# Optimization experiments

Hardware: AMD Instinct MI355X
Metric: run time of the kernel (lower is better)

Reference implementation:

```python
import jax, jax.numpy as jnp
import numpy as np

A, B, D, H, O = 64, 4096, 50, 192, 3

def _xavier(key, shape, gain=0.5):
    fan_in, fan_out = shape[-1], shape[-2]
    limit = gain * np.sqrt(6.0 / (fan_in + fan_out))
    return jax.random.uniform(key, shape, jnp.float32, -limit, limit)

def setup_inputs() -> dict:
    key = jax.random.key(0)
    ks = jax.random.split(key, 12)
    return {
        "x": jax.random.normal(ks[0], (B, D), jnp.float32),
        "input_norm_weight": _xavier(ks[1], (A, D)),
        "input_norm_bias": jnp.zeros((A, D), jnp.float32),
        "layer1_weight": _xavier(ks[2], (A, H, D)),
        "layer1_bias": jnp.zeros((A, H), jnp.float32),
        "layer2_weight": _xavier(ks[3], (A, H, H)),
        "layer2_bias": jnp.zeros((A, H), jnp.float32),
        "layer3_weight": _xavier(ks[4], (A, H, H)),
        "layer3_bias": jnp.zeros((A, H), jnp.float32),
        "output_weight": _xavier(ks[5], (A, O, H)),
        "output_bias": jnp.zeros((A, O), jnp.float32),
        "skip1_weight": _xavier(ks[6], (A, H, D)),
        "skip1_bias": jnp.zeros((A, H), jnp.float32),
        "skip2_weight": _xavier(ks[7], (A, H, H)),
        "skip2_bias": jnp.zeros((A, H), jnp.float32),
        "hidden_norm_weight": _xavier(ks[8], (A, H)),
        "hidden_norm_bias": jnp.zeros((A, H), jnp.float32),
    }

def reference(x, input_norm_weight, input_norm_bias,
              layer1_weight, layer1_bias, layer2_weight, layer2_bias,
              layer3_weight, layer3_bias, output_weight, output_bias,
              skip1_weight, skip1_bias, skip2_weight, skip2_bias,
              hidden_norm_weight, hidden_norm_bias):
    # NOTE: the vectorized ensemble's "norms" are affine-only (no mean/var), per source.
    # x: [B, D] -> broadcast over agents: [A, B, D]
    x_norm = x[None, :, :] * input_norm_weight[:, None, :] + input_norm_bias[:, None, :]
    gelu = lambda t: jax.nn.gelu(t, approximate=False)  # torch F.gelu exact
    # per-agent GEMMs: [A,B,in] x [A,out,in] -> [A,B,out]
    h1 = gelu(jnp.einsum('abi,ahi->abh', x_norm, layer1_weight) + layer1_bias[:, None, :]) \
         + jnp.einsum('abi,ahi->abh', x_norm, skip1_weight) + skip1_bias[:, None, :]
    h2 = gelu(jnp.einsum('abi,ahi->abh', h1, layer2_weight) + layer2_bias[:, None, :]) \
         + jnp.einsum('abi,ahi->abh', h1, skip2_weight) + skip2_bias[:, None, :]
    h3 = jnp.einsum('abi,ahi->abh', h2, layer3_weight) + layer3_bias[:, None, :] + h2
    h3 = h3 * hidden_norm_weight[:, None, :] + hidden_norm_bias[:, None, :]
    logits = jnp.einsum('abh,aoh->abo', h3, output_weight) + output_bias[:, None, :]
    return logits  # [A, B, O]
```

## Files before the change

### kernel.cpp

```cpp
#include <hip/hip_runtime.h>
#include <math.h>

#define A_N 64
#define B_N 4096
#define D_N 50
#define H_N 192
#define O_N 3

typedef __attribute__((ext_vector_type(8))) __bf16 bf16x8;
typedef __attribute__((ext_vector_type(4))) __bf16 bf16x4;
typedef __attribute__((ext_vector_type(4))) float f32x4;

#define W1_OFF   0
#define S1_OFF   786432
#define W2_OFF   1572864
#define S2_OFF   3932160
#define W3_OFF   6291456
#define OW_OFF   8650752
#define WS_ELEMS 8847360

#if __has_builtin(__builtin_amdgcn_rcpf)
#define FRCP(x) __builtin_amdgcn_rcpf(x)
#else
#define FRCP(x) (1.0f / (x))
#endif
#if __has_builtin(__builtin_amdgcn_exp2f)
#define FEXP2(x) __builtin_amdgcn_exp2f(x)
#else
#define FEXP2(x) exp2f(x)
#endif

__device__ __forceinline__ float gelu_f(float xx) {
    float t  = 0.70710678118654752440f * xx;
    float at = fabsf(t);
    float k  = FRCP(fmaf(0.3275911f, at, 1.0f));
    float p  = fmaf(k, 1.061405429f, -1.453152027f);
    p = fmaf(k, p, 1.421413741f);
    p = fmaf(k, p, -0.284496736f);
    p = fmaf(k, p, 0.254829592f);
    p = p * k;
    float e  = FEXP2(t * t * -1.44269504088896340736f);
    float er = fmaf(-p, e, 1.0f);
    er = (t < 0.f) ? -er : er;
    return 0.5f * xx * (1.0f + er);
}

__global__ __launch_bounds__(256)
void prep_kernel(const float* __restrict__ w1, const float* __restrict__ s1,
                 const float* __restrict__ w2, const float* __restrict__ s2,
                 const float* __restrict__ w3, const float* __restrict__ ow,
                 __bf16* __restrict__ ws) {
    __shared__ __bf16 T[192 * 72];
    const int b   = blockIdx.x;
    const int tid = threadIdx.x;

    if (b < 384) {
        int m = b / 128;
        int r = b % 128; int a = r >> 1; int half = r & 1;
        const float* src = ((m == 0) ? w2 : (m == 1) ? s2 : w3) + (size_t)a * 36864;
        __bf16* dst = ws + ((m == 0) ? W2_OFF : (m == 1) ? S2_OFF : W3_OFF) + (size_t)a * 36864;
        for (int rc = half * 3; rc < half * 3 + 3; ++rc) {
            #pragma unroll
            for (int i = 0; i < 6; ++i) {
                int f4 = i * 256 + tid;
                int row = f4 / 48, kc = (f4 % 48) * 4;
                f32x4 v = *(const f32x4*)(src + (size_t)(rc * 32 + row) * 192 + kc);
                bf16x4 o;
                #pragma unroll
                for (int j = 0; j < 4; ++j) o[j] = (__bf16)v[j];
                *(bf16x4*)(T + row * 200 + kc) = o;
            }
            __syncthreads();
            #pragma unroll
            for (int i = 0; i < 3; ++i) {
                int fr = i * 256 + tid;
                int f = fr >> 6, lane = fr & 63;
                int ntl = f / 6, ks = f % 6;
                int n = ntl * 16 + (lane & 15), k = ks * 32 + (lane >> 4) * 8;
                bf16x8 v = *(const bf16x8*)(T + n * 200 + k);
                *(bf16x8*)(dst + ((size_t)(rc * 2 + ntl) * 6 + ks) * 512 + lane * 8) = v;
            }
            __syncthreads();
        }
    } else if (b < 512) {
        int r = b - 384; int m = r >> 6; int a = r & 63;
        const float* src = (m ? s1 : w1) + (size_t)a * 9600;
        __bf16* dst = ws + (m ? S1_OFF : W1_OFF) + (size_t)a * 12288;
        for (int e = tid; e < 192 * 72; e += 256) T[e] = (__bf16)0.f;
        __syncthreads();
        for (int e = tid; e < 9600; e += 256) {
            int row = e / 50, k = e - row * 50;
            T[row * 72 + k] = (__bf16)src[e];
        }
        __syncthreads();
        #pragma unroll
        for (int i = 0; i < 6; ++i) {
            int fr = i * 256 + tid;
            int f = fr >> 6, lane = fr & 63;
            int nt = f >> 1, ks = f & 1;
            int n = nt * 16 + (lane & 15), k = ks * 32 + (lane >> 4) * 8;
            bf16x8 v = *(const bf16x8*)(T + n * 72 + k);
            *(bf16x8*)(dst + (size_t)(nt * 2 + ks) * 512 + lane * 8) = v;
        }
    } else {
        int r = b - 512;
        #pragma unroll
        for (int i = 0; i < 8; ++i) {
            int fr = (r * 8 + i) * 256 + tid;
            int a = fr / 384, rem = fr - a * 384;
            int ks = rem >> 6, lane = rem & 63;
            int n = lane & 15, k = ks * 32 + (lane >> 4) * 8;
            bf16x8 v;
            if (n < O_N) {
                const float* p = ow + ((size_t)a * O_N + n) * H_N + k;
                f32x4 f0 = *(const f32x4*)p, f1 = *(const f32x4*)(p + 4);
                #pragma unroll
                for (int j = 0; j < 4; ++j) { v[j] = (__bf16)f0[j]; v[4 + j] = (__bf16)f1[j]; }
            } else {
                #pragma unroll
                for (int j = 0; j < 8; ++j) v[j] = (__bf16)0.f;
            }
            *(bf16x8*)(ws + OW_OFF + (size_t)a * 3072 + ks * 512 + lane * 8) = v;
        }
    }
}

#define MFMA(a, b, c) __builtin_amdgcn_mfma_f32_16x16x32_bf16((a), (b), (c), 0, 0, 0)

__global__ __launch_bounds__(256, 3)
void srek_mfma(const float* __restrict__ x,
               const float* __restrict__ inw, const float* __restrict__ inb,
               const float* __restrict__ b1,  const float* __restrict__ b2,
               const float* __restrict__ b3,  const float* __restrict__ s1b,
               const float* __restrict__ s2b, const float* __restrict__ hnw,
               const float* __restrict__ hnb, const float* __restrict__ ob,
               const __bf16* __restrict__ ws, float* __restrict__ out) {
    __shared__ __bf16 Xs[64 * 72];
    __shared__ __bf16 Hs[64 * 200];

    const int bid  = blockIdx.x;
    const int slot = bid >> 3;
    const int tile = slot & 63;
    const int a    = ((bid & 7) << 3) | (slot >> 6);
    const int row0 = tile * 64;

    const int tid  = threadIdx.x;
    const int lane = tid & 63;
    const int wv   = tid >> 6;
    const int ln   = lane & 15;
    const int quad = lane >> 4;
    const int aH   = a * H_N;
    const int c0   = wv * 48;
    const int l8   = lane * 8;
    const int f3   = wv * 3;

    const __bf16* W1 = ws + W1_OFF + (size_t)a * 12288;
    const __bf16* S1 = ws + S1_OFF + (size_t)a * 12288;
    const __bf16* W2 = ws + W2_OFF + (size_t)a * 36864;
    const __bf16* S2 = ws + S2_OFF + (size_t)a * 36864;
    const __bf16* W3 = ws + W3_OFF + (size_t)a * 36864;
    const __bf16* OWp= ws + OW_OFF + (size_t)a * 3072;

    bf16x8 nxt[6];
    f32x4 accT[12], accS[12], h2f[12];
    const f32x4 zero = {0.f, 0.f, 0.f, 0.f};

    #pragma unroll
    for (int t = 0; t < 3; ++t) {
        nxt[t]     = *(const bf16x8*)(W1 + ((f3 + t) * 2 + 0) * 512 + l8);
        nxt[3 + t] = *(const bf16x8*)(S1 + ((f3 + t) * 2 + 0) * 512 + l8);
    }

    for (int e = tid; e < 64 * 64; e += 256) {
        int r = e >> 6, k = e & 63;
        float v = 0.f;
        if (k < D_N) v = x[(size_t)(row0 + r) * D_N + k] * inw[a * D_N + k] + inb[a * D_N + k];
        Xs[r * 72 + k] = (__bf16)v;
    }

    auto compute_dual = [&](const __bf16* As, int pitch, int ks,
                            const bf16x8* cw, const bf16x8* cs) {
        #pragma unroll
        for (int mt = 0; mt < 4; ++mt) {
            bf16x8 av = *(const bf16x8*)(As + (mt * 16 + ln) * pitch + ks * 32 + quad * 8);
            #pragma unroll
            for (int t = 0; t < 3; ++t) {
                accT[mt * 3 + t] = MFMA(cw[t], av, accT[mt * 3 + t]);
                accS[mt * 3 + t] = MFMA(cs[t], av, accS[mt * 3 + t]);
            }
        }
    };
    auto compute_single = [&](int ks, const bf16x8* cw) {
        #pragma unroll
        for (int mt = 0; mt < 4; ++mt) {
            bf16x8 av = *(const bf16x8*)(Hs + (mt * 16 + ln) * 200 + ks * 32 + quad * 8);
            #pragma unroll
            for (int t = 0; t < 3; ++t)
                accT[mt * 3 + t] = MFMA(cw[t], av, accT[mt * 3 + t]);
        }
    };

    #pragma unroll
    for (int i = 0; i < 12; ++i) { accT[i] = zero; accS[i] = zero; }
    __syncthreads();

    {
        bf16x8 cw[3], cs[3];
        #pragma unroll
        for (int t = 0; t < 3; ++t) { cw[t] = nxt[t]; cs[t] = nxt[3 + t]; }
        #pragma unroll
        for (int t = 0; t < 3; ++t) {
            nxt[t]     = *(const bf16x8*)(W1 + ((f3 + t) * 2 + 1) * 512 + l8);
            nxt[3 + t] = *(const bf16x8*)(S1 + ((f3 + t) * 2 + 1) * 512 + l8);
        }
        compute_dual(Xs, 72, 0, cw, cs);
        #pragma unroll
        for (int t = 0; t < 3; ++t) { cw[t] = nxt[t]; cs[t] = nxt[3 + t]; }
        #pragma unroll
        for (int t = 0; t < 3; ++t) {
            nxt[t]     = *(const bf16x8*)(W2 + ((f3 + t) * 6 + 0) * 512 + l8);
            nxt[3 + t] = *(const bf16x8*)(S2 + ((f3 + t) * 6 + 0) * 512 + l8);
        }
        compute_dual(Xs, 72, 1, cw, cs);
    }
    #pragma unroll
    for (int t = 0; t < 3; ++t) {
        int colb = c0 + t * 16 + quad * 4;
        f32x4 bb = *(const f32x4*)(b1 + aH + colb);
        f32x4 sb = *(const f32x4*)(s1b + aH + colb);
        #pragma unroll
        for (int mt = 0; mt < 4; ++mt) {
            bf16x4 o;
            #pragma unroll
            for (int rg = 0; rg < 4; ++rg)
                o[rg] = (__bf16)(gelu_f(accT[mt * 3 + t][rg] + bb[rg]) + accS[mt * 3 + t][rg] + sb[rg]);
            *(bf16x4*)(Hs + (mt * 16 + ln) * 200 + colb) = o;
        }
    }
    #pragma unroll
    for (int i = 0; i < 12; ++i) { accT[i] = zero; accS[i] = zero; }
    __syncthreads();

    #pragma unroll
    for (int ks = 0; ks < 6; ++ks) {
        bf16x8 cw[3], cs[3];
        #pragma unroll
        for (int t = 0; t < 3; ++t) { cw[t] = nxt[t]; cs[t] = nxt[3 + t]; }
        if (ks < 5) {
            #pragma unroll
            for (int t = 0; t < 3; ++t) {
                nxt[t]     = *(const bf16x8*)(W2 + ((f3 + t) * 6 + ks + 1) * 512 + l8);
                nxt[3 + t] = *(const bf16x8*)(S2 + ((f3 + t) * 6 + ks + 1) * 512 + l8);
            }
        } else {
            #pragma unroll
            for (int t = 0; t < 3; ++t)
                nxt[t] = *(const bf16x8*)(W3 + ((f3 + t) * 6 + 0) * 512 + l8);
        }
        compute_dual(Hs, 200, ks, cw, cs);
    }
    #pragma unroll
    for (int t = 0; t < 3; ++t) {
        int colb = c0 + t * 16 + quad * 4;
        f32x4 bb = *(const f32x4*)(b2 + aH + colb);
        f32x4 sb = *(const f32x4*)(s2b + aH + colb);
        #pragma unroll
        for (int mt = 0; mt < 4; ++mt)
            #pragma unroll
            for (int rg = 0; rg < 4; ++rg)
                h2f[mt * 3 + t][rg] = gelu_f(accT[mt * 3 + t][rg] + bb[rg]) + accS[mt * 3 + t][rg] + sb[rg];
    }
    #pragma unroll
    for (int i = 0; i < 12; ++i) accT[i] = zero;
    __syncthreads();
    #pragma unroll
    for (int t = 0; t < 3; ++t) {
        int colb = c0 + t * 16 + quad * 4;
        #pragma unroll
        for (int mt = 0; mt < 4; ++mt) {
            bf16x4 o;
            #pragma unroll
            for (int rg = 0; rg < 4; ++rg) o[rg] = (__bf16)h2f[mt * 3 + t][rg];
            *(bf16x4*)(Hs + (mt * 16 + ln) * 200 + colb) = o;
        }
    }
    __syncthreads();

    bf16x8 ow6[6];
    #pragma unroll
    for (int ks = 0; ks < 6; ++ks) {
        bf16x8 cw[3];
        #pragma unroll
        for (int t = 0; t < 3; ++t) cw[t] = nxt[t];
        if (ks < 5) {
            #pragma unroll
            for (int t = 0; t < 3; ++t)
                nxt[t] = *(const bf16x8*)(W3 + ((f3 + t) * 6 + ks + 1) * 512 + l8);
        } else {
            #pragma unroll
            for (int kk = 0; kk < 6; ++kk)
                ow6[kk] = *(const bf16x8*)(OWp + kk * 512 + l8);
        }
        compute_single(ks, cw);
    }
    #pragma unroll
    for (int t = 0; t < 3; ++t) {
        int colb = c0 + t * 16 + quad * 4;
        f32x4 b3v = *(const f32x4*)(b3  + aH + colb);
        f32x4 nwv = *(const f32x4*)(hnw + aH + colb);
        f32x4 nbv = *(const f32x4*)(hnb + aH + colb);
        #pragma unroll
        for (int mt = 0; mt < 4; ++mt)
            #pragma unroll
            for (int rg = 0; rg < 4; ++rg)
                h2f[mt * 3 + t][rg] = fmaf(accT[mt * 3 + t][rg] + b3v[rg] + h2f[mt * 3 + t][rg],
                                           nwv[rg], nbv[rg]);
    }
    __syncthreads();
    #pragma unroll
    for (int t = 0; t < 3; ++t) {
        int colb = c0 + t * 16 + quad * 4;
        #pragma unroll
        for (int mt = 0; mt < 4; ++mt) {
            bf16x4 o;
            #pragma unroll
            for (int rg = 0; rg < 4; ++rg) o[rg] = (__bf16)h2f[mt * 3 + t][rg];
            *(bf16x4*)(Hs + (mt * 16 + ln) * 200 + colb) = o;
        }
    }
    __syncthreads();

    {
        f32x4 acco = zero;
        #pragma unroll
        for (int ks = 0; ks < 6; ++ks) {
            bf16x8 av = *(const bf16x8*)(Hs + (wv * 16 + ln) * 200 + ks * 32 + quad * 8);
            acco = MFMA(ow6[ks], av, acco);
        }
        if (quad == 0) {
            float* po = out + ((size_t)a * B_N + row0 + wv * 16 + ln) * O_N;
            po[0] = acco[0] + ob[a * O_N + 0];
            po[1] = acco[1] + ob[a * O_N + 1];
            po[2] = acco[2] + ob[a * O_N + 2];
        }
    }
}

extern "C" void kernel_launch(void* const* d_in, const int* in_sizes, int n_in,
                              void* d_out, int out_size, void* d_ws, size_t ws_size,
                              hipStream_t stream) {
    const float* x   = (const float*)d_in[0];
    const float* inw = (const float*)d_in[1];
    const float* inb = (const float*)d_in[2];
    const float* w1  = (const float*)d_in[3];
    const float* b1  = (const float*)d_in[4];
    const float* w2  = (const float*)d_in[5];
    const float* b2  = (const float*)d_in[6];
    const float* w3  = (const float*)d_in[7];
    const float* b3  = (const float*)d_in[8];
    const float* ow  = (const float*)d_in[9];
    const float* ob  = (const float*)d_in[10];
    const float* s1w = (const float*)d_in[11];
    const float* s1b = (const float*)d_in[12];
    const float* s2w = (const float*)d_in[13];
    const float* s2b = (const float*)d_in[14];
    const float* hnw = (const float*)d_in[15];
    const float* hnb = (const float*)d_in[16];

    __bf16* ws = (__bf16*)d_ws;

    prep_kernel<<<dim3(524), dim3(256), 0, stream>>>(w1, s1w, w2, s2w, w3, ow, ws);

    srek_mfma<<<dim3(A_N * (B_N / 64)), dim3(256), 0, stream>>>(
        x, inw, inb, b1, b2, b3, s1b, s2b, hnw, hnb, ob, ws, (float*)d_out);
}
```

Measured before the change: 246.5 us.

## Fold skip GEMMs into one accumulator set and raise occupancy to four blocks

The main kernel drops the separate accT, accS and h2f accumulator arrays and keeps a single set of 12 accumulators. It runs the main-weight pass, applies bias and GELU in place, then accumulates the skip-weight pass and the residual on top. This cuts register pressure so launch bounds can rise from 3 to 4 blocks per CU, at the cost of reading the activation fragments from LDS twice per layer. The prep kernel is also split into one block per 32-row chunk, giving more parallel blocks and dropping the inner loop and the extra barriers.

```diff
diff --git a/kernel.cpp b/kernel.cpp
--- a/kernel.cpp
+++ b/kernel.cpp
@@ -54,36 +54,35 @@
     const int b   = blockIdx.x;
     const int tid = threadIdx.x;
 
-    if (b < 384) {
-        int m = b / 128;
-        int r = b % 128; int a = r >> 1; int half = r & 1;
+    if (b < 1152) {
+        int m  = b / 384;
+        int r  = b % 384;
+        int a  = r / 6;
+        int rc = r % 6;
         const float* src = ((m == 0) ? w2 : (m == 1) ? s2 : w3) + (size_t)a * 36864;
         __bf16* dst = ws + ((m == 0) ? W2_OFF : (m == 1) ? S2_OFF : W3_OFF) + (size_t)a * 36864;
-        for (int rc = half * 3; rc < half * 3 + 3; ++rc) {
-            #pragma unroll
-            for (int i = 0; i < 6; ++i) {
-                int f4 = i * 256 + tid;
-                int row = f4 / 48, kc = (f4 % 48) * 4;
-                f32x4 v = *(const f32x4*)(src + (size_t)(rc * 32 + row) * 192 + kc);
-                bf16x4 o;
-                #pragma unroll
-                for (int j = 0; j < 4; ++j) o[j] = (__bf16)v[j];
-                *(bf16x4*)(T + row * 200 + kc) = o;
-            }
-            __syncthreads();
-            #pragma unroll
-            for (int i = 0; i < 3; ++i) {
-                int fr = i * 256 + tid;
-                int f = fr >> 6, lane = fr & 63;
-                int ntl = f / 6, ks = f % 6;
-                int n = ntl * 16 + (lane & 15), k = ks * 32 + (lane >> 4) * 8;
-                bf16x8 v = *(const bf16x8*)(T + n * 200 + k);
-                *(bf16x8*)(dst + ((size_t)(rc * 2 + ntl) * 6 + ks) * 512 + lane * 8) = v;
-            }
-            __syncthreads();
-        }
-    } else if (b < 512) {
-        int r = b - 384; int m = r >> 6; int a = r & 63;
+        #pragma unroll
+        for (int i = 0; i < 6; ++i) {
+            int f4 = i * 256 + tid;
+            int row = f4 / 48, kc = (f4 % 48) * 4;
+            f32x4 v = *(const f32x4*)(src + (size_t)(rc * 32 + row) * 192 + kc);
+            bf16x4 o;
+            #pragma unroll
+            for (int j = 0; j < 4; ++j) o[j] = (__bf16)v[j];
+            *(bf16x4*)(T + row * 200 + kc) = o;
+        }
+        __syncthreads();
+        #pragma unroll
+        for (int i = 0; i < 3; ++i) {
+            int fr = i * 256 + tid;
+            int f = fr >> 6, lane = fr & 63;
+            int ntl = f / 6, ks = f % 6;
+            int n = ntl * 16 + (lane & 15), k = ks * 32 + (lane >> 4) * 8;
+            bf16x8 v = *(const bf16x8*)(T + n * 200 + k);
+            *(bf16x8*)(dst + ((size_t)(rc * 2 + ntl) * 6 + ks) * 512 + lane * 8) = v;
+        }
+    } else if (b < 1280) {
+        int r = b - 1152; int m = r >> 6; int a = r & 63;
         const float* src = (m ? s1 : w1) + (size_t)a * 9600;
         __bf16* dst = ws + (m ? S1_OFF : W1_OFF) + (size_t)a * 12288;
         for (int e = tid; e < 192 * 72; e += 256) T[e] = (__bf16)0.f;
@@ -103,7 +102,7 @@
             *(bf16x8*)(dst + (size_t)(nt * 2 + ks) * 512 + lane * 8) = v;
         }
     } else {
-        int r = b - 512;
+        int r = b - 1280;
         #pragma unroll
         for (int i = 0; i < 8; ++i) {
             int fr = (r * 8 + i) * 256 + tid;
@@ -127,7 +126,7 @@
 
 #define MFMA(a, b, c) __builtin_amdgcn_mfma_f32_16x16x32_bf16((a), (b), (c), 0, 0, 0)
 
-__global__ __launch_bounds__(256, 3)
+__global__ __launch_bounds__(256, 4)
 void srek_mfma(const float* __restrict__ x,
                const float* __restrict__ inw, const float* __restrict__ inb,
                const float* __restrict__ b1,  const float* __restrict__ b2,
@@ -161,15 +160,56 @@
     const __bf16* W3 = ws + W3_OFF + (size_t)a * 36864;
     const __bf16* OWp= ws + OW_OFF + (size_t)a * 3072;
 
-    bf16x8 nxt[6];
-    f32x4 accT[12], accS[12], h2f[12];
+    bf16x8 nxt[3], cw[3], ow6[6];
+    f32x4 acc[12];
     const f32x4 zero = {0.f, 0.f, 0.f, 0.f};
 
-    #pragma unroll
-    for (int t = 0; t < 3; ++t) {
-        nxt[t]     = *(const bf16x8*)(W1 + ((f3 + t) * 2 + 0) * 512 + l8);
-        nxt[3 + t] = *(const bf16x8*)(S1 + ((f3 + t) * 2 + 0) * 512 + l8);
-    }
+    auto ldw3 = [&](const __bf16* base, int KS, int ks) {
+        #pragma unroll
+        for (int t = 0; t < 3; ++t)
+            nxt[t] = *(const bf16x8*)(base + ((f3 + t) * KS + ks) * 512 + l8);
+    };
+    auto take = [&]() {
+        #pragma unroll
+        for (int t = 0; t < 3; ++t) cw[t] = nxt[t];
+    };
+    auto pass = [&](const __bf16* As, int pitch, int ks) {
+        #pragma unroll
+        for (int mt = 0; mt < 4; ++mt) {
+            bf16x8 av = *(const bf16x8*)(As + (mt * 16 + ln) * pitch + ks * 32 + quad * 8);
+            #pragma unroll
+            for (int t = 0; t < 3; ++t)
+                acc[mt * 3 + t] = MFMA(cw[t], av, acc[mt * 3 + t]);
+        }
+    };
+    auto gelu_xform = [&](const float* bp, const float* sp) {
+        #pragma unroll
+        for (int t = 0; t < 3; ++t) {
+            int colb = c0 + t * 16 + quad * 4;
+            f32x4 bb = *(const f32x4*)(bp + aH + colb);
+            f32x4 sb = *(const f32x4*)(sp + aH + colb);
+            #pragma unroll
+            for (int mt = 0; mt < 4; ++mt)
+                #pragma unroll
+                for (int rg = 0; rg < 4; ++rg)
+                    acc[mt * 3 + t][rg] = gelu_f(acc[mt * 3 + t][rg] + bb[rg]) + sb[rg];
+        }
+    };
+    auto store_acc_bf16 = [&]() {
+        #pragma unroll
+        for (int t = 0; t < 3; ++t) {
+            int colb = c0 + t * 16 + quad * 4;
+            #pragma unroll
+            for (int mt = 0; mt < 4; ++mt) {
+                bf16x4 o;
+                #pragma unroll
+                for (int rg = 0; rg < 4; ++rg) o[rg] = (__bf16)acc[mt * 3 + t][rg];
+                *(bf16x4*)(Hs + (mt * 16 + ln) * 200 + colb) = o;
+            }
+        }
+    };
+
+    ldw3(W1, 2, 0);
 
     for (int e = tid; e < 64 * 64; e += 256) {
         int r = e >> 6, k = e & 63;
@@ -177,157 +217,71 @@
         if (k < D_N) v = x[(size_t)(row0 + r) * D_N + k] * inw[a * D_N + k] + inb[a * D_N + k];
         Xs[r * 72 + k] = (__bf16)v;
     }
-
-    auto compute_dual = [&](const __bf16* As, int pitch, int ks,
-                            const bf16x8* cw, const bf16x8* cs) {
-        #pragma unroll
-        for (int mt = 0; mt < 4; ++mt) {
-            bf16x8 av = *(const bf16x8*)(As + (mt * 16 + ln) * pitch + ks * 32 + quad * 8);
-            #pragma unroll
-            for (int t = 0; t < 3; ++t) {
-                accT[mt * 3 + t] = MFMA(cw[t], av, accT[mt * 3 + t]);
-                accS[mt * 3 + t] = MFMA(cs[t], av, accS[mt * 3 + t]);
-            }
-        }
-    };
-    auto compute_single = [&](int ks, const bf16x8* cw) {
-        #pragma unroll
-        for (int mt = 0; mt < 4; ++mt) {
-            bf16x8 av = *(const bf16x8*)(Hs + (mt * 16 + ln) * 200 + ks * 32 + quad * 8);
-            #pragma unroll
-            for (int t = 0; t < 3; ++t)
-                accT[mt * 3 + t] = MFMA(cw[t], av, accT[mt * 3 + t]);
-        }
-    };
-
-    #pragma unroll
-    for (int i = 0; i < 12; ++i) { accT[i] = zero; accS[i] = zero; }
-    __syncthreads();
-
-    {
-        bf16x8 cw[3], cs[3];
-        #pragma unroll
-        for (int t = 0; t < 3; ++t) { cw[t] = nxt[t]; cs[t] = nxt[3 + t]; }
-        #pragma unroll
-        for (int t = 0; t < 3; ++t) {
-            nxt[t]     = *(const bf16x8*)(W1 + ((f3 + t) * 2 + 1) * 512 + l8);
-            nxt[3 + t] = *(const bf16x8*)(S1 + ((f3 + t) * 2 + 1) * 512 + l8);
-        }
-        compute_dual(Xs, 72, 0, cw, cs);
-        #pragma unroll
-        for (int t = 0; t < 3; ++t) { cw[t] = nxt[t]; cs[t] = nxt[3 + t]; }
-        #pragma unroll
-        for (int t = 0; t < 3; ++t) {
-            nxt[t]     = *(const bf16x8*)(W2 + ((f3 + t) * 6 + 0) * 512 + l8);
-            nxt[3 + t] = *(const bf16x8*)(S2 + ((f3 + t) * 6 + 0) * 512 + l8);
-        }
-        compute_dual(Xs, 72, 1, cw, cs);
-    }
+    #pragma unroll
+    for (int i = 0; i < 12; ++i) acc[i] = zero;
+    __syncthreads();
+
+    take(); ldw3(W1, 2, 1); pass(Xs, 72, 0);
+    take(); ldw3(S1, 2, 0); pass(Xs, 72, 1);
+    gelu_xform(b1, s1b);
+    take(); ldw3(S1, 2, 1); pass(Xs, 72, 0);
+    take(); ldw3(W2, 6, 0); pass(Xs, 72, 1);
+    store_acc_bf16();
+    #pragma unroll
+    for (int i = 0; i < 12; ++i) acc[i] = zero;
+    __syncthreads();
+
+    #pragma unroll
+    for (int ks = 0; ks < 6; ++ks) {
+        take();
+        if (ks < 5) ldw3(W2, 6, ks + 1); else ldw3(S2, 6, 0);
+        pass(Hs, 200, ks);
+    }
+    gelu_xform(b2, s2b);
+    #pragma unroll
+    for (int ks = 0; ks < 6; ++ks) {
+        take();
+        if (ks < 5) ldw3(S2, 6, ks + 1); else ldw3(W3, 6, 0);
+        pass(Hs, 200, ks);
+    }
+    __syncthreads();
+    store_acc_bf16();
     #pragma unroll
     for (int t = 0; t < 3; ++t) {
         int colb = c0 + t * 16 + quad * 4;
-        f32x4 bb = *(const f32x4*)(b1 + aH + colb);
-        f32x4 sb = *(const f32x4*)(s1b + aH + colb);
-        #pragma unroll
-        for (int mt = 0; mt < 4; ++mt) {
-            bf16x4 o;
+        f32x4 b3v = *(const f32x4*)(b3 + aH + colb);
+        #pragma unroll
+        for (int mt = 0; mt < 4; ++mt)
             #pragma unroll
             for (int rg = 0; rg < 4; ++rg)
-                o[rg] = (__bf16)(gelu_f(accT[mt * 3 + t][rg] + bb[rg]) + accS[mt * 3 + t][rg] + sb[rg]);
-            *(bf16x4*)(Hs + (mt * 16 + ln) * 200 + colb) = o;
-        }
-    }
-    #pragma unroll
-    for (int i = 0; i < 12; ++i) { accT[i] = zero; accS[i] = zero; }
+                acc[mt * 3 + t][rg] += b3v[rg];
+    }
     __syncthreads();
 
     #pragma unroll
     for (int ks = 0; ks < 6; ++ks) {
-        bf16x8 cw[3], cs[3];
-        #pragma unroll
-        for (int t = 0; t < 3; ++t) { cw[t] = nxt[t]; cs[t] = nxt[3 + t]; }
-        if (ks < 5) {
-            #pragma unroll
-            for (int t = 0; t < 3; ++t) {
-                nxt[t]     = *(const bf16x8*)(W2 + ((f3 + t) * 6 + ks + 1) * 512 + l8);
-                nxt[3 + t] = *(const bf16x8*)(S2 + ((f3 + t) * 6 + ks + 1) * 512 + l8);
-            }
-        } else {
-            #pragma unroll
-            for (int t = 0; t < 3; ++t)
-                nxt[t] = *(const bf16x8*)(W3 + ((f3 + t) * 6 + 0) * 512 + l8);
-        }
-        compute_dual(Hs, 200, ks, cw, cs);
+        take();
+        if (ks < 5) ldw3(W3, 6, ks + 1);
+        else {
+            #pragma unroll
+            for (int kk = 0; kk < 6; ++kk)
+                ow6[kk] = *(const bf16x8*)(OWp + kk * 512 + l8);
+        }
+        pass(Hs, 200, ks);
     }
     #pragma unroll
     for (int t = 0; t < 3; ++t) {
         int colb = c0 + t * 16 + quad * 4;
-        f32x4 bb = *(const f32x4*)(b2 + aH + colb);
-        f32x4 sb = *(const f32x4*)(s2b + aH + colb);
-        #pragma unroll
-        for (int mt = 0; mt < 4; ++mt)
-            #pragma unroll
-            for (int rg = 0; rg < 4; ++rg)
-                h2f[mt * 3 + t][rg] = gelu_f(accT[mt * 3 + t][rg] + bb[rg]) + accS[mt * 3 + t][rg] + sb[rg];
-    }
-    #pragma unroll
-    for (int i = 0; i < 12; ++i) accT[i] = zero;
-    __syncthreads();
-    #pragma unroll
-    for (int t = 0; t < 3; ++t) {
-        int colb = c0 + t * 16 + quad * 4;
-        #pragma unroll
-        for (int mt = 0; mt < 4; ++mt) {
-            bf16x4 o;
-            #pragma unroll
-            for (int rg = 0; rg < 4; ++rg) o[rg] = (__bf16)h2f[mt * 3 + t][rg];
-            *(bf16x4*)(Hs + (mt * 16 + ln) * 200 + colb) = o;
-        }
-    }
-    __syncthreads();
-
-    bf16x8 ow6[6];
-    #pragma unroll
-    for (int ks = 0; ks < 6; ++ks) {
-        bf16x8 cw[3];
-        #pragma unroll
-        for (int t = 0; t < 3; ++t) cw[t] = nxt[t];
-        if (ks < 5) {
-            #pragma unroll
-            for (int t = 0; t < 3; ++t)
-                nxt[t] = *(const bf16x8*)(W3 + ((f3 + t) * 6 + ks + 1) * 512 + l8);
-        } else {
-            #pragma unroll
-            for (int kk = 0; kk < 6; ++kk)
-                ow6[kk] = *(const bf16x8*)(OWp + kk * 512 + l8);
-        }
-        compute_single(ks, cw);
-    }
-    #pragma unroll
-    for (int t = 0; t < 3; ++t) {
-        int colb = c0 + t * 16 + quad * 4;
-        f32x4 b3v = *(const f32x4*)(b3  + aH + colb);
         f32x4 nwv = *(const f32x4*)(hnw + aH + colb);
         f32x4 nbv = *(const f32x4*)(hnb + aH + colb);
         #pragma unroll
         for (int mt = 0; mt < 4; ++mt)
             #pragma unroll
             for (int rg = 0; rg < 4; ++rg)
-                h2f[mt * 3 + t][rg] = fmaf(accT[mt * 3 + t][rg] + b3v[rg] + h2f[mt * 3 + t][rg],
-                                           nwv[rg], nbv[rg]);
-    }
-    __syncthreads();
-    #pragma unroll
-    for (int t = 0; t < 3; ++t) {
-        int colb = c0 + t * 16 + quad * 4;
-        #pragma unroll
-        for (int mt = 0; mt < 4; ++mt) {
-            bf16x4 o;
-            #pragma unroll
-            for (int rg = 0; rg < 4; ++rg) o[rg] = (__bf16)h2f[mt * 3 + t][rg];
-            *(bf16x4*)(Hs + (mt * 16 + ln) * 200 + colb) = o;
-        }
-    }
+                acc[mt * 3 + t][rg] = fmaf(acc[mt * 3 + t][rg], nwv[rg], nbv[rg]);
+    }
+    __syncthreads();
+    store_acc_bf16();
     __syncthreads();
 
     {
@@ -369,7 +323,7 @@
 
     __bf16* ws = (__bf16*)d_ws;
 
-    prep_kernel<<<dim3(524), dim3(256), 0, stream>>>(w1, s1w, w2, s2w, w3, ow, ws);
+    prep_kernel<<<dim3(1292), dim3(256), 0, stream>>>(w1, s1w, w2, s2w, w3, ow, ws);
 
     srek_mfma<<<dim3(A_N * (B_N / 64)), dim3(256), 0, stream>>>(
         x, inw, inb, b1, b2, b3, s1b, s2b, hnw, hnb, ob, ws, (float*)d_out);
```

After: 306.5 us. +24.3%, slower.

## Store activations in MFMA fragment-major LDS layout and split prep blocks

Applied to the files above, without the earlier changes.

Xs and Hs switch from padded row-major LDS tiles to an MFMA fragment-major layout. Each lane's A-operand read becomes one contiguous 16-byte load at lane*8, which is meant to remove bank conflicts and index arithmetic in the inner MFMA loops. The epilogue writes now scatter into that fragment layout through a shared helper. Separately, the weight-prep kernel gives each 32-row chunk its own block (1292 blocks instead of 524), adding parallelism and dropping a loop and one barrier per chunk.

```diff
diff --git a/kernel.cpp b/kernel.cpp
--- a/kernel.cpp
+++ b/kernel.cpp
@@ -54,36 +54,35 @@
     const int b   = blockIdx.x;
     const int tid = threadIdx.x;
 
-    if (b < 384) {
-        int m = b / 128;
-        int r = b % 128; int a = r >> 1; int half = r & 1;
+    if (b < 1152) {
+        int m  = b / 384;
+        int r  = b % 384;
+        int a  = r / 6;
+        int rc = r % 6;
         const float* src = ((m == 0) ? w2 : (m == 1) ? s2 : w3) + (size_t)a * 36864;
         __bf16* dst = ws + ((m == 0) ? W2_OFF : (m == 1) ? S2_OFF : W3_OFF) + (size_t)a * 36864;
-        for (int rc = half * 3; rc < half * 3 + 3; ++rc) {
-            #pragma unroll
-            for (int i = 0; i < 6; ++i) {
-                int f4 = i * 256 + tid;
-                int row = f4 / 48, kc = (f4 % 48) * 4;
-                f32x4 v = *(const f32x4*)(src + (size_t)(rc * 32 + row) * 192 + kc);
-                bf16x4 o;
-                #pragma unroll
-                for (int j = 0; j < 4; ++j) o[j] = (__bf16)v[j];
-                *(bf16x4*)(T + row * 200 + kc) = o;
-            }
-            __syncthreads();
-            #pragma unroll
-            for (int i = 0; i < 3; ++i) {
-                int fr = i * 256 + tid;
-                int f = fr >> 6, lane = fr & 63;
-                int ntl = f / 6, ks = f % 6;
-                int n = ntl * 16 + (lane & 15), k = ks * 32 + (lane >> 4) * 8;
-                bf16x8 v = *(const bf16x8*)(T + n * 200 + k);
-                *(bf16x8*)(dst + ((size_t)(rc * 2 + ntl) * 6 + ks) * 512 + lane * 8) = v;
-            }
-            __syncthreads();
-        }
-    } else if (b < 512) {
-        int r = b - 384; int m = r >> 6; int a = r & 63;
+        #pragma unroll
+        for (int i = 0; i < 6; ++i) {
+            int f4 = i * 256 + tid;
+            int row = f4 / 48, kc = (f4 % 48) * 4;
+            f32x4 v = *(const f32x4*)(src + (size_t)(rc * 32 + row) * 192 + kc);
+            bf16x4 o;
+            #pragma unroll
+            for (int j = 0; j < 4; ++j) o[j] = (__bf16)v[j];
+            *(bf16x4*)(T + row * 200 + kc) = o;
+        }
+        __syncthreads();
+        #pragma unroll
+        for (int i = 0; i < 3; ++i) {
+            int fr = i * 256 + tid;
+            int f = fr >> 6, lane = fr & 63;
+            int ntl = f / 6, ks = f % 6;
+            int n = ntl * 16 + (lane & 15), k = ks * 32 + (lane >> 4) * 8;
+            bf16x8 v = *(const bf16x8*)(T + n * 200 + k);
+            *(bf16x8*)(dst + ((size_t)(rc * 2 + ntl) * 6 + ks) * 512 + lane * 8) = v;
+        }
+    } else if (b < 1280) {
+        int r = b - 1152; int m = r >> 6; int a = r & 63;
         const float* src = (m ? s1 : w1) + (size_t)a * 9600;
         __bf16* dst = ws + (m ? S1_OFF : W1_OFF) + (size_t)a * 12288;
         for (int e = tid; e < 192 * 72; e += 256) T[e] = (__bf16)0.f;
@@ -103,7 +102,7 @@
             *(bf16x8*)(dst + (size_t)(nt * 2 + ks) * 512 + lane * 8) = v;
         }
     } else {
-        int r = b - 512;
+        int r = b - 1280;
         #pragma unroll
         for (int i = 0; i < 8; ++i) {
             int fr = (r * 8 + i) * 256 + tid;
@@ -135,8 +134,8 @@
                const float* __restrict__ s2b, const float* __restrict__ hnw,
                const float* __restrict__ hnb, const float* __restrict__ ob,
                const __bf16* __restrict__ ws, float* __restrict__ out) {
-    __shared__ __bf16 Xs[64 * 72];
-    __shared__ __bf16 Hs[64 * 200];
+    __shared__ __bf16 Xs[8 * 512];
+    __shared__ __bf16 Hs[24 * 512];
 
     const int bid  = blockIdx.x;
     const int slot = bid >> 3;
@@ -171,18 +170,24 @@
         nxt[3 + t] = *(const bf16x8*)(S1 + ((f3 + t) * 2 + 0) * 512 + l8);
     }
 
-    for (int e = tid; e < 64 * 64; e += 256) {
-        int r = e >> 6, k = e & 63;
+    for (int e = tid; e < 8 * 512; e += 256) {
+        int j   = e & 7;
+        int lnn = (e >> 3) & 15;
+        int qd  = (e >> 7) & 3;
+        int kss = (e >> 9) & 1;
+        int mtt = (e >> 10) & 3;
+        int r = mtt * 16 + lnn;
+        int k = kss * 32 + qd * 8 + j;
         float v = 0.f;
         if (k < D_N) v = x[(size_t)(row0 + r) * D_N + k] * inw[a * D_N + k] + inb[a * D_N + k];
-        Xs[r * 72 + k] = (__bf16)v;
-    }
-
-    auto compute_dual = [&](const __bf16* As, int pitch, int ks,
+        Xs[e] = (__bf16)v;
+    }
+
+    auto compute_dual = [&](const __bf16* As, int KS, int ks,
                             const bf16x8* cw, const bf16x8* cs) {
         #pragma unroll
         for (int mt = 0; mt < 4; ++mt) {
-            bf16x8 av = *(const bf16x8*)(As + (mt * 16 + ln) * pitch + ks * 32 + quad * 8);
+            bf16x8 av = *(const bf16x8*)(As + (mt * KS + ks) * 512 + l8);
             #pragma unroll
             for (int t = 0; t < 3; ++t) {
                 accT[mt * 3 + t] = MFMA(cw[t], av, accT[mt * 3 + t]);
@@ -193,10 +198,25 @@
     auto compute_single = [&](int ks, const bf16x8* cw) {
         #pragma unroll
         for (int mt = 0; mt < 4; ++mt) {
-            bf16x8 av = *(const bf16x8*)(Hs + (mt * 16 + ln) * 200 + ks * 32 + quad * 8);
+            bf16x8 av = *(const bf16x8*)(Hs + (mt * 6 + ks) * 512 + l8);
             #pragma unroll
             for (int t = 0; t < 3; ++t)
                 accT[mt * 3 + t] = MFMA(cw[t], av, accT[mt * 3 + t]);
+        }
+    };
+    auto store_fragmajor = [&](const f32x4* src) {
+        #pragma unroll
+        for (int t = 0; t < 3; ++t) {
+            int ks2 = (3 * wv + t) >> 1;
+            int qp  = (6 * wv + 2 * t + (quad >> 1)) & 3;
+            int off = (qp * 16 + ln) * 8 + (quad & 1) * 4;
+            #pragma unroll
+            for (int mt = 0; mt < 4; ++mt) {
+                bf16x4 o;
+                #pragma unroll
+                for (int rg = 0; rg < 4; ++rg) o[rg] = (__bf16)src[mt * 3 + t][rg];
+                *(bf16x4*)(Hs + (mt * 6 + ks2) * 512 + off) = o;
+            }
         }
     };
 
@@ -213,7 +233,7 @@
             nxt[t]     = *(const bf16x8*)(W1 + ((f3 + t) * 2 + 1) * 512 + l8);
             nxt[3 + t] = *(const bf16x8*)(S1 + ((f3 + t) * 2 + 1) * 512 + l8);
         }
-        compute_dual(Xs, 72, 0, cw, cs);
+        compute_dual(Xs, 2, 0, cw, cs);
         #pragma unroll
         for (int t = 0; t < 3; ++t) { cw[t] = nxt[t]; cs[t] = nxt[3 + t]; }
         #pragma unroll
@@ -221,7 +241,7 @@
             nxt[t]     = *(const bf16x8*)(W2 + ((f3 + t) * 6 + 0) * 512 + l8);
             nxt[3 + t] = *(const bf16x8*)(S2 + ((f3 + t) * 6 + 0) * 512 + l8);
         }
-        compute_dual(Xs, 72, 1, cw, cs);
+        compute_dual(Xs, 2, 1, cw, cs);
     }
     #pragma unroll
     for (int t = 0; t < 3; ++t) {
@@ -229,14 +249,12 @@
         f32x4 bb = *(const f32x4*)(b1 + aH + colb);
         f32x4 sb = *(const f32x4*)(s1b + aH + colb);
         #pragma unroll
-        for (int mt = 0; mt < 4; ++mt) {
-            bf16x4 o;
+        for (int mt = 0; mt < 4; ++mt)
             #pragma unroll
             for (int rg = 0; rg < 4; ++rg)
-                o[rg] = (__bf16)(gelu_f(accT[mt * 3 + t][rg] + bb[rg]) + accS[mt * 3 + t][rg] + sb[rg]);
-            *(bf16x4*)(Hs + (mt * 16 + ln) * 200 + colb) = o;
-        }
-    }
+                h2f[mt * 3 + t][rg] = gelu_f(accT[mt * 3 + t][rg] + bb[rg]) + accS[mt * 3 + t][rg] + sb[rg];
+    }
+    store_fragmajor(h2f);
     #pragma unroll
     for (int i = 0; i < 12; ++i) { accT[i] = zero; accS[i] = zero; }
     __syncthreads();
@@ -257,7 +275,7 @@
             for (int t = 0; t < 3; ++t)
                 nxt[t] = *(const bf16x8*)(W3 + ((f3 + t) * 6 + 0) * 512 + l8);
         }
-        compute_dual(Hs, 200, ks, cw, cs);
+        compute_dual(Hs, 6, ks, cw, cs);
     }
     #pragma unroll
     for (int t = 0; t < 3; ++t) {
@@ -273,17 +291,7 @@
     #pragma unroll
     for (int i = 0; i < 12; ++i) accT[i] = zero;
     __syncthreads();
-    #pragma unroll
-    for (int t = 0; t < 3; ++t) {
-        int colb = c0 + t * 16 + quad * 4;
-        #pragma unroll
-        for (int mt = 0; mt < 4; ++mt) {
-            bf16x4 o;
-            #pragma unroll
-            for (int rg = 0; rg < 4; ++rg) o[rg] = (__bf16)h2f[mt * 3 + t][rg];
-            *(bf16x4*)(Hs + (mt * 16 + ln) * 200 + colb) = o;
-        }
-    }
+    store_fragmajor(h2f);
     __syncthreads();
 
     bf16x8 ow6[6];
@@ -317,24 +325,14 @@
                                            nwv[rg], nbv[rg]);
     }
     __syncthreads();
-    #pragma unroll
-    for (int t = 0; t < 3; ++t) {
-        int colb = c0 + t * 16 + quad * 4;
-        #pragma unroll
-        for (int mt = 0; mt < 4; ++mt) {
-            bf16x4 o;
-            #pragma unroll
-            for (int rg = 0; rg < 4; ++rg) o[rg] = (__bf16)h2f[mt * 3 + t][rg];
-            *(bf16x4*)(Hs + (mt * 16 + ln) * 200 + colb) = o;
-        }
-    }
+    store_fragmajor(h2f);
     __syncthreads();
 
     {
         f32x4 acco = zero;
         #pragma unroll
         for (int ks = 0; ks < 6; ++ks) {
-            bf16x8 av = *(const bf16x8*)(Hs + (wv * 16 + ln) * 200 + ks * 32 + quad * 8);
+            bf16x8 av = *(const bf16x8*)(Hs + (wv * 6 + ks) * 512 + l8);
             acco = MFMA(ow6[ks], av, acco);
         }
         if (quad == 0) {
@@ -369,7 +367,7 @@
 
     __bf16* ws = (__bf16*)d_ws;
 
-    prep_kernel<<<dim3(524), dim3(256), 0, stream>>>(w1, s1w, w2, s2w, w3, ow, ws);
+    prep_kernel<<<dim3(1292), dim3(256), 0, stream>>>(w1, s1w, w2, s2w, w3, ow, ws);
 
     srek_mfma<<<dim3(A_N * (B_N / 64)), dim3(256), 0, stream>>>(
         x, inw, inb, b1, b2, b3, s1b, s2b, hnw, hnb, ob, ws, (float*)d_out);
```

Measured after the change: 226.3 us. 1.09x faster.
